# Kernel tuning notes

Measured on AMD Instinct MI355X. Metric: run time of the kernel, lower is better.

Reference implementation:

```python
import jax, jax.numpy as jnp
import numpy as np

DIM = 128
HEADS = 8
DH = DIM // HEADS
WIN = (4, 4, 4)
TOPK = 4
EPS = 1e-6


def _ln(x, g, b):
    mu = jnp.mean(x, -1, keepdims=True)
    var = jnp.mean((x - mu) ** 2, -1, keepdims=True)
    return (x - mu) * jax.lax.rsqrt(var + EPS) * g + b


def _win3d(x, p1, p2, p3):
    # x: [B,S,H,W,C] -> [B, p1*p2*p3, Ms, Mh, Mw, C]
    B, S, H, W, C = x.shape
    Ms, Mh, Mw = S // p1, H // p2, W // p3
    x = x.reshape(B, p1, Ms, p2, Mh, p3, Mw, C)
    x = x.transpose(0, 1, 3, 5, 2, 4, 6, 7)
    return x.reshape(B, p1 * p2 * p3, Ms, Mh, Mw, C)


def setup_inputs() -> dict:
    key = jax.random.key(0)
    ks = jax.random.split(key, 20)

    def lin(k, din, dout):
        return jax.random.normal(k, (din, dout), jnp.float32) * 0.02

    return {
        "x_in": jax.random.normal(ks[0], (2, 128, 16, 32, 32), jnp.float32),
        "x_g_in": jax.random.normal(ks[1], (2, 128, 8, 16, 16), jnp.float32),
        # Atten (global branch)
        "qkv_w": lin(ks[2], DIM, 3 * DIM), "qkv_b": jnp.zeros((3 * DIM,), jnp.float32),
        "proj_w": lin(ks[3], DIM, DIM), "proj_b": jnp.zeros((DIM,), jnp.float32),
        # shared LayerNorm (self.norm1 is reused everywhere in the original)
        "ln_g": jnp.ones((DIM,), jnp.float32), "ln_b": jnp.zeros((DIM,), jnp.float32),
        # mlp (global branch FFN)
        "mlp_w1": lin(ks[4], DIM, 4 * DIM), "mlp_b1": jnp.zeros((4 * DIM,), jnp.float32),
        "mlp_w2": lin(ks[5], 4 * DIM, DIM), "mlp_b2": jnp.zeros((DIM,), jnp.float32),
        # TopkRouting
        "rq_w": lin(ks[6], DIM, DIM), "rq_b": jnp.zeros((DIM,), jnp.float32),
        "rk_w": lin(ks[7], DIM, DIM), "rk_b": jnp.zeros((DIM,), jnp.float32),
        # fused qkv over concatenated local+gathered-global tokens
        "gqkv_w": lin(ks[8], DIM, 3 * DIM), "gqkv_b": jnp.zeros((3 * DIM,), jnp.float32),
        "wo_w": lin(ks[9], DIM, DIM), "wo_b": jnp.zeros((DIM,), jnp.float32),
        # mlp2 (local branch FFN)
        "mlp2_w1": lin(ks[10], DIM, 4 * DIM), "mlp2_b1": jnp.zeros((4 * DIM,), jnp.float32),
        "mlp2_w2": lin(ks[11], 4 * DIM, DIM), "mlp2_b2": jnp.zeros((DIM,), jnp.float32),
    }


def reference(x_in, x_g_in, qkv_w, qkv_b, proj_w, proj_b, ln_g, ln_b,
              mlp_w1, mlp_b1, mlp_w2, mlp_b2, rq_w, rq_b, rk_w, rk_b,
              gqkv_w, gqkv_b, wo_w, wo_b, mlp2_w1, mlp2_b1, mlp2_w2, mlp2_b2):
    B, C, S, H, W = x_in.shape
    Ms, Mh, Mw = WIN
    p1, p2, p3 = S // Ms, H // Mh, W // Mw  # pads are zero for these shapes
    nw, w3l = p1 * p2 * p3, Ms * Mh * Mw
    scale = DIM ** -0.5  # BiLevelRoutingAttention.scale = dim**-0.5 (not per-head)

    x = jnp.transpose(x_in, (0, 2, 3, 4, 1))  # [B,S,H,W,C]
    shortcut_l = _win3d(x, p1, p2, p3).reshape(B, nw, w3l, C)

    # ---- global branch: full self-attention + FFN ----
    _, _, gS, gH, gW = x_g_in.shape
    gN = gS * gH * gW
    xg = jnp.transpose(x_g_in, (0, 2, 3, 4, 1)).reshape(B, gN, C)
    h = _ln(xg, ln_g, ln_b)
    qkv = (h @ qkv_w + qkv_b).reshape(B, gN, 3, HEADS, DH).transpose(2, 0, 3, 1, 4)
    q, k, v = qkv[0], qkv[1], qkv[2]
    a = jax.nn.softmax(jnp.einsum('bhnd,bhmd->bhnm', q, k) * DH ** -0.5, axis=-1)
    o = jnp.einsum('bhnm,bhmd->bhnd', a, v).transpose(0, 2, 1, 3).reshape(B, gN, C)
    xg = (o @ proj_w + proj_b) + xg
    xg4 = xg.reshape(B, gS, gH, gW, C)
    h = _ln(xg4, ln_g, ln_b)
    xg4 = xg4 + (jax.nn.gelu(h @ mlp_w1 + mlp_b1, approximate=False) @ mlp_w2 + mlp_b2)

    # ---- top-k window routing ----
    swg = _win3d(xg4, p1, p2, p3)  # [B,nw,gMs,gMh,gMw,C]
    w3g = swg.shape[2] * swg.shape[3] * swg.shape[4]
    g_win = swg.mean((2, 3, 4))  # [B,nw,C]
    qh = g_win @ rq_w + rq_b
    kh = g_win @ rk_w + rk_b
    logit = jnp.einsum('bnc,bmc->bnm', qh * scale, kh)
    _tvals, tidx = jax.lax.top_k(logit, TOPK)  # r_weight is computed but unused in the original forward

    # gather top-k global windows' tokens per local window
    gflat = swg.reshape(B, nw, w3g, C)
    gath = jax.vmap(lambda kv, idx: kv[idx])(gflat, tidx)  # [B,nw,topk,w3g,C]
    sc = jnp.concatenate([shortcut_l, gath.reshape(B, nw, TOPK * w3g, C)], axis=2)
    w3 = w3l + TOPK * w3g

    # ---- local+routed attention over concatenated tokens ----
    qkvp = _ln(sc, ln_g, ln_b) @ gqkv_w + gqkv_b
    qp, kp, vp = jnp.split(qkvp, 3, axis=-1)
    qp = qp.reshape(B, nw, w3, HEADS, DH)
    kp = kp.reshape(B, nw, w3, HEADS, DH)
    vp = vp.reshape(B, nw, w3, HEADS, DH)
    aw = jax.nn.softmax(jnp.einsum('bnqhd,bnkhd->bnhqk', qp * scale, kp), axis=-1)
    out = jnp.einsum('bnhqk,bnkhd->bnqhd', aw, vp).reshape(B, nw, w3, C)

    l = out[:, :, :w3l] @ wo_w + wo_b + shortcut_l
    l = l.reshape(B, p1, p2, p3, Ms, Mh, Mw, C).transpose(0, 1, 4, 2, 5, 3, 6, 7).reshape(B, S, H, W, C)
    l = l + (jax.nn.gelu(_ln(l, ln_g, ln_b) @ mlp2_w1 + mlp2_b1, approximate=False) @ mlp2_w2 + mlp2_b2)

    l_out = jnp.transpose(l, (0, 4, 1, 2, 3))
    g_out = jnp.transpose(xg4, (0, 4, 1, 2, 3))
    return (l_out, g_out)
```

## Files before the change

kernel.cpp:

```cpp
#include <hip/hip_runtime.h>
#include <hip/hip_bf16.h>
#include <math.h>

#define BATCH 2
#define CDIM 128
#define SS 16
#define HH_ 32
#define WW_ 32
#define NSP (SS*HH_*WW_)
#define GS 8
#define GH 16
#define GW 16
#define GN (GS*GH*GW)
#define HEADS 8
#define DH 16
#define NW 256
#define W3L 64
#define W3G 8
#define TOPK 4
#define W3 (W3L + TOPK*W3G)
#define LN_EPS 1e-6f
#define ROUTE_SCALE 0.08838834764831845f
#define GATTN_SCALE 0.25f

typedef short bshort8 __attribute__((ext_vector_type(8)));
typedef float f32x4 __attribute__((ext_vector_type(4)));

__device__ __forceinline__ unsigned short f2bf(float f) {
    unsigned int u = __float_as_uint(f);
    unsigned int r = (u + 0x7fffu + ((u >> 16) & 1u)) >> 16;
    return (unsigned short)r;
}
__device__ __forceinline__ float gelu_exact(float x) {
    return 0.5f * x * (1.0f + erff(x * 0.70710678118654752f));
}
__device__ __forceinline__ float shfl_sum32(float v) {
#pragma unroll
    for (int m = 16; m > 0; m >>= 1) v += __shfl_xor(v, m);
    return v;
}
__device__ __forceinline__ float shfl_sum16(float v) {
#pragma unroll
    for (int m = 8; m > 0; m >>= 1) v += __shfl_xor(v, m);
    return v;
}
__device__ __forceinline__ float shfl_sum8(float v) {
#pragma unroll
    for (int m = 4; m > 0; m >>= 1) v += __shfl_xor(v, m);
    return v;
}

__global__ __launch_bounds__(256) void k_wprep_all(const float* __restrict__ gqkv_w,
        const float* __restrict__ m2_w1, const float* __restrict__ m2_w2,
        const float* __restrict__ proj_w, const float* __restrict__ mlp_w1,
        const float* __restrict__ mlp_w2, const float* __restrict__ wo_w,
        const float* __restrict__ qkv_w,
        unsigned short* __restrict__ wt, unsigned short* __restrict__ w1t,
        unsigned short* __restrict__ w2t, unsigned short* __restrict__ projt,
        unsigned short* __restrict__ gw1t, unsigned short* __restrict__ gw2t,
        unsigned short* __restrict__ wot, unsigned short* __restrict__ qkvt) {
    int id = blockIdx.x * 256 + threadIdx.x;
    if (id < 49152) {
        int n = id >> 7, k = id & 127;
        float v = gqkv_w[k * 384 + n];
        if (n < 128) v *= ROUTE_SCALE;
        wt[id] = f2bf(v);
    } else if (id < 114688) {
        int i = id - 49152; int n = i >> 7, k = i & 127;
        w1t[i] = f2bf(m2_w1[k * 512 + n]);
    } else if (id < 180224) {
        int i = id - 114688; int n = i >> 9, k = i & 511;
        w2t[i] = f2bf(m2_w2[k * 128 + n]);
    } else if (id < 196608) {
        int i = id - 180224; int n = i >> 7, k = i & 127;
        projt[i] = f2bf(proj_w[k * 128 + n]);
    } else if (id < 262144) {
        int i = id - 196608; int n = i >> 7, k = i & 127;
        gw1t[i] = f2bf(mlp_w1[k * 512 + n]);
    } else if (id < 327680) {
        int i = id - 262144; int n = i >> 9, k = i & 511;
        gw2t[i] = f2bf(mlp_w2[k * 128 + n]);
    } else if (id < 344064) {
        int i = id - 327680; int n = i >> 7, k = i & 127;
        wot[i] = f2bf(wo_w[k * 128 + n]);
    } else {
        int i = id - 344064; int n = i >> 7, k = i & 127;
        float v = qkv_w[k * 384 + n];
        if (n < 128) v *= GATTN_SCALE;
        qkvt[i] = f2bf(v);
    }
}

__global__ __launch_bounds__(256) void k_gqkv_mfma(const float* __restrict__ xg_in,
        const unsigned short* __restrict__ qkvt, const float* __restrict__ qkv_b,
        const float* __restrict__ ln_g, const float* __restrict__ ln_b,
        float* __restrict__ xg, unsigned short* __restrict__ qgb,
        unsigned short* __restrict__ kgb, unsigned short* __restrict__ vgtb) {
    int blk = blockIdx.x; int b = blk >> 7; int n0 = (blk & 127) * 16;
    int t = threadIdx.x; int w = t >> 6; int lane = t & 63;
    int l15 = lane & 15, quad = lane >> 4;
    __shared__ __align__(16) float xs[16 * 132];
    __shared__ __align__(16) unsigned short h[16 * 136];
    f32x4 zero4 = {0.f, 0.f, 0.f, 0.f};

    {
        int c = t >> 1, j0 = (t & 1) * 8;
        const float* src = xg_in + ((size_t)(b * 128 + c)) * GN + n0 + j0;
        float4 v0 = *(const float4*)src;
        float4 v1 = *(const float4*)(src + 4);
        xs[(j0 + 0) * 132 + c] = v0.x; xs[(j0 + 1) * 132 + c] = v0.y;
        xs[(j0 + 2) * 132 + c] = v0.z; xs[(j0 + 3) * 132 + c] = v0.w;
        xs[(j0 + 4) * 132 + c] = v1.x; xs[(j0 + 5) * 132 + c] = v1.y;
        xs[(j0 + 6) * 132 + c] = v1.z; xs[(j0 + 7) * 132 + c] = v1.w;
    }
    __syncthreads();
    {
        int j = t >> 4, p = t & 15, c0 = p * 8;
        float vv[8]; float s1 = 0.f;
#pragma unroll
        for (int i = 0; i < 8; i++) { vv[i] = xs[j * 132 + c0 + i]; s1 += vv[i]; }
        s1 = shfl_sum16(s1);
        float mu = s1 * (1.0f / 128.0f);
        float s2 = 0.f;
#pragma unroll
        for (int i = 0; i < 8; i++) { float d = vv[i] - mu; s2 += d * d; }
        s2 = shfl_sum16(s2);
        float rs = rsqrtf(s2 * (1.0f / 128.0f) + LN_EPS);
        float* dst = xg + ((size_t)(b * GN) + n0 + j) * 128 + c0;
        *(float4*)dst = *(float4*)&vv[0];
        *(float4*)(dst + 4) = *(float4*)&vv[4];
        unsigned short hb[8];
#pragma unroll
        for (int i4 = 0; i4 < 2; i4++) {
            float4 g4 = *(const float4*)(ln_g + c0 + i4 * 4);
            float4 b4 = *(const float4*)(ln_b + c0 + i4 * 4);
            hb[i4 * 4 + 0] = f2bf((vv[i4 * 4 + 0] - mu) * rs * g4.x + b4.x);
            hb[i4 * 4 + 1] = f2bf((vv[i4 * 4 + 1] - mu) * rs * g4.y + b4.y);
            hb[i4 * 4 + 2] = f2bf((vv[i4 * 4 + 2] - mu) * rs * g4.z + b4.z);
            hb[i4 * 4 + 3] = f2bf((vv[i4 * 4 + 3] - mu) * rs * g4.w + b4.w);
        }
        *(ushort4*)&h[j * 136 + c0] = *(ushort4*)&hb[0];
        *(ushort4*)&h[j * 136 + c0 + 4] = *(ushort4*)&hb[4];
    }
    __syncthreads();

    bshort8 a[4];
#pragma unroll
    for (int ks = 0; ks < 4; ks++)
        a[ks] = *(const bshort8*)(h + l15 * 136 + ks * 32 + quad * 8);
    int bh_base = b * HEADS;
#pragma unroll
    for (int part = 0; part < 2; part++) {
#pragma unroll
        for (int which = 0; which < 2; which++) {
            int nt = 2 * w + which;
            int ncol = part * 128 + nt * 16;
            f32x4 acc = zero4;
#pragma unroll
            for (int ks = 0; ks < 4; ks++) {
                bshort8 bfr = *(const bshort8*)(qkvt + (size_t)(ncol + l15) * 128 + ks * 32 + quad * 8);
                acc = __builtin_amdgcn_mfma_f32_16x16x32_bf16(a[ks], bfr, acc, 0, 0, 0);
            }
            float bias = qkv_b[ncol + l15] * (part == 0 ? GATTN_SCALE : 1.f);
            unsigned short* dst = (part == 0) ? qgb : kgb;
#pragma unroll
            for (int r = 0; r < 4; r++)
                dst[((size_t)(bh_base + nt) * GN + n0 + quad * 4 + r) * DH + l15] = f2bf(acc[r] + bias);
        }
    }
#pragma unroll
    for (int which = 0; which < 2; which++) {
        int mtv = 2 * w + which;
        f32x4 acc = zero4;
#pragma unroll
        for (int ks = 0; ks < 4; ks++) {
            bshort8 aw = *(const bshort8*)(qkvt + (size_t)(256 + mtv * 16 + l15) * 128 + ks * 32 + quad * 8);
            acc = __builtin_amdgcn_mfma_f32_16x16x32_bf16(aw, a[ks], acc, 0, 0, 0);
        }
#pragma unroll
        for (int r = 0; r < 4; r++) {
            float bias = qkv_b[256 + mtv * 16 + quad * 4 + r];
            vgtb[((size_t)(bh_base + mtv) * DH + quad * 4 + r) * GN + n0 + l15] = f2bf(acc[r] + bias);
        }
    }
}

__global__ __launch_bounds__(256) void k_gattn_mfma(const unsigned short* __restrict__ qgb,
        const unsigned short* __restrict__ kgb, const unsigned short* __restrict__ vgtb,
        float* __restrict__ og) {
    int blk = blockIdx.x;
    int bh = blk >> 7; int qt = (blk & 127) << 4;
    int b = bh >> 3, hh = bh & 7;
    int t = threadIdx.x; int w = t >> 6; int lane = t & 63;
    int col = lane & 15, quad = lane >> 4;
    __shared__ __align__(16) unsigned short Pbuf[4 * 16 * 40];
    __shared__ float po[4][64][4];
    __shared__ float pl[4][64][4];

    bshort8 aq = {0, 0, 0, 0, 0, 0, 0, 0};
    if (quad < 2)
        aq = *(const bshort8*)(qgb + ((size_t)bh * GN + qt + col) * DH + quad * 8);

    f32x4 o = {0.f, 0.f, 0.f, 0.f};
    float lsum[4] = {0.f, 0.f, 0.f, 0.f};
    const unsigned short* kb = kgb + (size_t)bh * GN * DH;
    const unsigned short* vb = vgtb + (size_t)bh * DH * GN;
    unsigned short* pb = Pbuf + w * (16 * 40);
    int row0 = quad * 4;
    int kbeg = w * 512;
    for (int kc = kbeg; kc < kbeg + 512; kc += 32) {
        bshort8 bk0 = {0, 0, 0, 0, 0, 0, 0, 0};
        bshort8 bk1 = {0, 0, 0, 0, 0, 0, 0, 0};
        if (quad < 2) {
            bk0 = *(const bshort8*)(kb + (size_t)(kc + col) * DH + quad * 8);
            bk1 = *(const bshort8*)(kb + (size_t)(kc + 16 + col) * DH + quad * 8);
        }
        f32x4 z = {0.f, 0.f, 0.f, 0.f};
        f32x4 s0 = __builtin_amdgcn_mfma_f32_16x16x32_bf16(aq, bk0, z, 0, 0, 0);
        f32x4 s1 = __builtin_amdgcn_mfma_f32_16x16x32_bf16(aq, bk1, z, 0, 0, 0);
        float p0[4], p1[4];
#pragma unroll
        for (int r = 0; r < 4; r++) {
            p0[r] = __expf(s0[r]); p1[r] = __expf(s1[r]);
            lsum[r] += p0[r] + p1[r];
        }
#pragma unroll
        for (int r = 0; r < 4; r++) {
            pb[(row0 + r) * 40 + col] = f2bf(p0[r]);
            pb[(row0 + r) * 40 + 16 + col] = f2bf(p1[r]);
        }
        bshort8 pA = *(const bshort8*)(pb + col * 40 + quad * 8);
        bshort8 bv = *(const bshort8*)(vb + (size_t)col * GN + kc + quad * 8);
        o = __builtin_amdgcn_mfma_f32_16x16x32_bf16(pA, bv, o, 0, 0, 0);
    }
#pragma unroll
    for (int r = 0; r < 4; r++) {
        float v = lsum[r];
        v += __shfl_xor(v, 1); v += __shfl_xor(v, 2);
        v += __shfl_xor(v, 4); v += __shfl_xor(v, 8);
        lsum[r] = v;
    }
#pragma unroll
    for (int r = 0; r < 4; r++) { po[w][lane][r] = o[r]; pl[w][lane][r] = lsum[r]; }
    __syncthreads();
    if (w == 0) {
#pragma unroll
        for (int r = 0; r < 4; r++) {
            float os = po[0][lane][r] + po[1][lane][r] + po[2][lane][r] + po[3][lane][r];
            float ls = pl[0][lane][r] + pl[1][lane][r] + pl[2][lane][r] + pl[3][lane][r];
            og[((size_t)(b * GN) + qt + quad * 4 + r) * 128 + hh * 16 + col] = os / ls;
        }
    }
}

__global__ __launch_bounds__(256) void k_gmlp_mfma(const float* __restrict__ og,
        const float* __restrict__ xg,
        const unsigned short* __restrict__ projt, const float* __restrict__ proj_b,
        const float* __restrict__ ln_g, const float* __restrict__ ln_b,
        const unsigned short* __restrict__ gw1t, const float* __restrict__ b1,
        const unsigned short* __restrict__ gw2t, const float* __restrict__ b2,
        float* __restrict__ xg4, float* __restrict__ gout) {
    int blk = blockIdx.x; int b = blk >> 7; int n0g = (blk & 127) * 16;
    int t = threadIdx.x; int w = t >> 6; int lane = t & 63;
    int l15 = lane & 15, quad = lane >> 4;
    __shared__ __align__(16) unsigned short ao[16 * 136];
    __shared__ __align__(16) float xs[16 * 132];
    __shared__ __align__(16) unsigned short h[16 * 136];
    __shared__ __align__(16) unsigned short h1[16 * 520];
    float* of32 = (float*)h1;
    f32x4 zero4 = {0.f, 0.f, 0.f, 0.f};

    {
        int j = t >> 4, p = t & 15, c0 = p * 8;
        size_t base = ((size_t)(b * GN) + n0g + j) * 128 + c0;
        float4 v0 = *(const float4*)(og + base);
        float4 v1 = *(const float4*)(og + base + 4);
        ushort4 u0 = { f2bf(v0.x), f2bf(v0.y), f2bf(v0.z), f2bf(v0.w) };
        ushort4 u1 = { f2bf(v1.x), f2bf(v1.y), f2bf(v1.z), f2bf(v1.w) };
        *(ushort4*)&ao[j * 136 + c0] = u0;
        *(ushort4*)&ao[j * 136 + c0 + 4] = u1;
        *(float4*)&xs[j * 132 + c0] = *(const float4*)(xg + base);
        *(float4*)&xs[j * 132 + c0 + 4] = *(const float4*)(xg + base + 4);
    }
    __syncthreads();

    {
        bshort8 a[4];
#pragma unroll
        for (int ks = 0; ks < 4; ks++)
            a[ks] = *(const bshort8*)(ao + l15 * 136 + ks * 32 + quad * 8);
#pragma unroll
        for (int nt = 0; nt < 2; nt++) {
            int n0 = w * 32 + nt * 16;
            f32x4 acc = zero4;
#pragma unroll
            for (int ks = 0; ks < 4; ks++) {
                bshort8 bfr = *(const bshort8*)(projt + (n0 + l15) * 128 + ks * 32 + quad * 8);
                acc = __builtin_amdgcn_mfma_f32_16x16x32_bf16(a[ks], bfr, acc, 0, 0, 0);
            }
            float bias = proj_b[n0 + l15];
#pragma unroll
            for (int r = 0; r < 4; r++) {
                int m = quad * 4 + r;
                xs[m * 132 + n0 + l15] += acc[r] + bias;
            }
        }
    }
    __syncthreads();

    {
        int j = t >> 4, p = t & 15, c0 = p * 8;
        float vv[8]; float s1 = 0.f;
#pragma unroll
        for (int i = 0; i < 8; i++) { vv[i] = xs[j * 132 + c0 + i]; s1 += vv[i]; }
        s1 = shfl_sum16(s1);
        float mu = s1 * (1.0f / 128.0f);
        float s2 = 0.f;
#pragma unroll
        for (int i = 0; i < 8; i++) { float d = vv[i] - mu; s2 += d * d; }
        s2 = shfl_sum16(s2);
        float rs = rsqrtf(s2 * (1.0f / 128.0f) + LN_EPS);
        unsigned short hb[8];
#pragma unroll
        for (int i4 = 0; i4 < 2; i4++) {
            float4 g4 = *(const float4*)(ln_g + c0 + i4 * 4);
            float4 b4 = *(const float4*)(ln_b + c0 + i4 * 4);
            hb[i4 * 4 + 0] = f2bf((vv[i4 * 4 + 0] - mu) * rs * g4.x + b4.x);
            hb[i4 * 4 + 1] = f2bf((vv[i4 * 4 + 1] - mu) * rs * g4.y + b4.y);
            hb[i4 * 4 + 2] = f2bf((vv[i4 * 4 + 2] - mu) * rs * g4.z + b4.z);
            hb[i4 * 4 + 3] = f2bf((vv[i4 * 4 + 3] - mu) * rs * g4.w + b4.w);
        }
        *(ushort4*)&h[j * 136 + c0] = *(ushort4*)&hb[0];
        *(ushort4*)&h[j * 136 + c0 + 4] = *(ushort4*)&hb[4];
    }
    __syncthreads();

    {
        bshort8 a[4];
#pragma unroll
        for (int ks = 0; ks < 4; ks++)
            a[ks] = *(const bshort8*)(h + l15 * 136 + ks * 32 + quad * 8);
#pragma unroll
        for (int nt = 0; nt < 8; nt++) {
            int n0 = w * 128 + nt * 16;
            f32x4 acc = zero4;
#pragma unroll
            for (int ks = 0; ks < 4; ks++) {
                bshort8 bfr = *(const bshort8*)(gw1t + (size_t)(n0 + l15) * 128 + ks * 32 + quad * 8);
                acc = __builtin_amdgcn_mfma_f32_16x16x32_bf16(a[ks], bfr, acc, 0, 0, 0);
            }
            float bias = b1[n0 + l15];
#pragma unroll
            for (int r = 0; r < 4; r++)
                h1[(quad * 4 + r) * 520 + n0 + l15] = f2bf(gelu_exact(acc[r] + bias));
        }
    }
    __syncthreads();

    f32x4 acc2[2]; acc2[0] = zero4; acc2[1] = zero4;
#pragma unroll 4
    for (int ks = 0; ks < 16; ks++) {
        bshort8 a = *(const bshort8*)(h1 + l15 * 520 + ks * 32 + quad * 8);
#pragma unroll
        for (int nt = 0; nt < 2; nt++) {
            int n0 = w * 32 + nt * 16;
            bshort8 bfr = *(const bshort8*)(gw2t + (size_t)(n0 + l15) * 512 + ks * 32 + quad * 8);
            acc2[nt] = __builtin_amdgcn_mfma_f32_16x16x32_bf16(a, bfr, acc2[nt], 0, 0, 0);
        }
    }
    __syncthreads();

    {
#pragma unroll
        for (int nt = 0; nt < 2; nt++) {
            int n0 = w * 32 + nt * 16;
            float bias = b2[n0 + l15];
#pragma unroll
            for (int r = 0; r < 4; r++) {
                int m = quad * 4 + r;
                float ov = xs[m * 132 + n0 + l15] + acc2[nt][r] + bias;
                of32[m * 132 + n0 + l15] = ov;
                xg4[((size_t)(b * GN) + n0g + m) * 128 + n0 + l15] = ov;
            }
        }
    }
    __syncthreads();

    {
        int cw = t >> 1, hf = t & 1, j0 = hf * 8;
        float* dst = gout + ((size_t)(b * 128 + cw)) * GN + n0g + j0;
#pragma unroll
        for (int i4 = 0; i4 < 2; i4++) {
            float4 ov = { of32[(j0 + i4 * 4 + 0) * 132 + cw], of32[(j0 + i4 * 4 + 1) * 132 + cw],
                          of32[(j0 + i4 * 4 + 2) * 132 + cw], of32[(j0 + i4 * 4 + 3) * 132 + cw] };
            *(float4*)(dst + i4 * 4) = ov;
        }
    }
}

__global__ void k_routing_qk(const float* __restrict__ xg4,
                             const float* __restrict__ rq_w, const float* __restrict__ rq_b,
                             const float* __restrict__ rk_w, const float* __restrict__ rk_b,
                             float* __restrict__ qh, float* __restrict__ kh) {
    int wid = blockIdx.x; int b = wid / NW, n = wid % NW;
    int c = threadIdx.x;
    int i1 = n / 64, i2 = (n / 8) % 8, i3 = n % 8;
    __shared__ float g[CDIM];
    float s = 0.f;
#pragma unroll
    for (int j = 0; j < W3G; j++) {
        int ds = j >> 2, dh = (j >> 1) & 1, dw = j & 1;
        int gi = ((i1 * 2 + ds) * GH + (i2 * 2 + dh)) * GW + (i3 * 2 + dw);
        s += xg4[((size_t)(b * GN + gi)) * CDIM + c];
    }
    g[c] = s * (1.0f / W3G);
    __syncthreads();
    float aq = rq_b[c], ak = rk_b[c];
    for (int k = 0; k < CDIM; k++) { float gv = g[k]; aq = fmaf(gv, rq_w[k * CDIM + c], aq); ak = fmaf(gv, rk_w[k * CDIM + c], ak); }
    qh[(size_t)wid * CDIM + c] = aq;
    kh[(size_t)wid * CDIM + c] = ak;
}

__global__ void k_topk(const float* __restrict__ qh, const float* __restrict__ kh,
                       int* __restrict__ tidx) {
    int wid = blockIdx.x; int b = wid / NW;
    int m = threadIdx.x;
    __shared__ float q[CDIM];
    __shared__ float lv[NW];
    __shared__ int li[NW];
    if (m < CDIM) q[m] = qh[(size_t)wid * CDIM + m] * ROUTE_SCALE;
    __syncthreads();
    float acc = 0.f;
    const float* kr = kh + ((size_t)b * NW + m) * CDIM;
    for (int k = 0; k < CDIM; k++) acc = fmaf(q[k], kr[k], acc);
#pragma unroll
    for (int sel = 0; sel < TOPK; sel++) {
        lv[m] = acc; li[m] = m; __syncthreads();
#pragma unroll
        for (int s = 128; s > 0; s >>= 1) {
            if (m < s) {
                if (lv[m + s] > lv[m] || (lv[m + s] == lv[m] && li[m + s] < li[m])) {
                    lv[m] = lv[m + s]; li[m] = li[m + s];
                }
            }
            __syncthreads();
        }
        int best = li[0]; __syncthreads();
        if (m == best) acc = -1e30f;
        if (m == 0) tidx[wid * TOPK + sel] = best;
    }
}

__global__ __launch_bounds__(256) void k_lnsc_local(const float* __restrict__ x_in,
        const float* __restrict__ ln_g, const float* __restrict__ ln_b,
        unsigned short* __restrict__ lnsc) {
    int blk = blockIdx.x;
    int wt = blk & 1; int hh = (blk >> 1) & 31; int s = (blk >> 6) & 15; int b = blk >> 10;
    int w0 = wt * 16;
    int t = threadIdx.x;
    __shared__ float tile[16][132];
    {
        int c = t >> 1; int wq = (t & 1) * 8;
        const float* src = x_in + (((size_t)(b * 128 + c) * SS + s)) * 1024 + hh * 32 + w0 + wq;
        float4 v0 = *(const float4*)src;
        float4 v1 = *(const float4*)(src + 4);
        tile[wq + 0][c] = v0.x; tile[wq + 1][c] = v0.y; tile[wq + 2][c] = v0.z; tile[wq + 3][c] = v0.w;
        tile[wq + 4][c] = v1.x; tile[wq + 5][c] = v1.y; tile[wq + 6][c] = v1.z; tile[wq + 7][c] = v1.w;
    }
    __syncthreads();
    int w = t >> 4; int j = t & 15;
    float vals[8];
    float s1 = 0.f;
#pragma unroll
    for (int i = 0; i < 8; i++) { vals[i] = tile[w][j * 8 + i]; s1 += vals[i]; }
    s1 = shfl_sum16(s1);
    float mu = s1 * (1.0f / 128.0f);
    float s2 = 0.f;
#pragma unroll
    for (int i = 0; i < 8; i++) { float d = vals[i] - mu; s2 += d * d; }
    s2 = shfl_sum16(s2);
    float rs = rsqrtf(s2 * (1.0f / 128.0f) + LN_EPS);
    float4 g0 = *(const float4*)(ln_g + j * 8);
    float4 g1 = *(const float4*)(ln_g + j * 8 + 4);
    float4 b0 = *(const float4*)(ln_b + j * 8);
    float4 b1 = *(const float4*)(ln_b + j * 8 + 4);
    float gv[8] = { g0.x, g0.y, g0.z, g0.w, g1.x, g1.y, g1.z, g1.w };
    float bv[8] = { b0.x, b0.y, b0.z, b0.w, b1.x, b1.y, b1.z, b1.w };
    int ww = w0 + w;
    int n = (s >> 2) * 64 + (hh >> 2) * 8 + (ww >> 2);
    int slot = (s & 3) * 16 + (hh & 3) * 4 + (ww & 3);
    unsigned short* dst = lnsc + ((size_t)(b * NW + n) * W3 + slot) * 128 + j * 8;
    ushort4 u0, u1;
    u0.x = f2bf((vals[0] - mu) * rs * gv[0] + bv[0]);
    u0.y = f2bf((vals[1] - mu) * rs * gv[1] + bv[1]);
    u0.z = f2bf((vals[2] - mu) * rs * gv[2] + bv[2]);
    u0.w = f2bf((vals[3] - mu) * rs * gv[3] + bv[3]);
    u1.x = f2bf((vals[4] - mu) * rs * gv[4] + bv[4]);
    u1.y = f2bf((vals[5] - mu) * rs * gv[5] + bv[5]);
    u1.z = f2bf((vals[6] - mu) * rs * gv[6] + bv[6]);
    u1.w = f2bf((vals[7] - mu) * rs * gv[7] + bv[7]);
    *(ushort4*)dst = u0;
    *(ushort4*)(dst + 4) = u1;
}

__global__ __launch_bounds__(256) void k_lnsc_gath(const float* __restrict__ xg4,
        const int* __restrict__ tidx,
        const float* __restrict__ ln_g, const float* __restrict__ ln_b,
        unsigned short* __restrict__ lnsc) {
    int blk = blockIdx.x;
    int kk = blk & 3; int wn = blk >> 2;
    int b = wn >> 8;
    int g = tidx[wn * TOPK + kk];
    int gi1 = g >> 6, gi2 = (g >> 3) & 7, gi3 = g & 7;
    int t = threadIdx.x; int j = t >> 5, lj = t & 31;
    int ds = j >> 2, dh = (j >> 1) & 1, dw = j & 1;
    int gi = ((gi1 * 2 + ds) * GH + (gi2 * 2 + dh)) * GW + (gi3 * 2 + dw);
    float4 v = *(const float4*)(xg4 + ((size_t)(b * GN + gi)) * 128 + lj * 4);
    float s1 = shfl_sum32(v.x + v.y + v.z + v.w);
    float mu = s1 * (1.0f / 128.0f);
    float d0 = v.x - mu, d1 = v.y - mu, d2 = v.z - mu, d3 = v.w - mu;
    float s2 = shfl_sum32(d0 * d0 + d1 * d1 + d2 * d2 + d3 * d3);
    float rs = rsqrtf(s2 * (1.0f / 128.0f) + LN_EPS);
    float4 g4 = *(const float4*)(ln_g + lj * 4);
    float4 b4 = *(const float4*)(ln_b + lj * 4);
    ushort4 u;
    u.x = f2bf(d0 * rs * g4.x + b4.x);
    u.y = f2bf(d1 * rs * g4.y + b4.y);
    u.z = f2bf(d2 * rs * g4.z + b4.z);
    u.w = f2bf(d3 * rs * g4.w + b4.w);
    *(ushort4*)(lnsc + ((size_t)wn * W3 + 64 + kk * 8 + j) * 128 + lj * 4) = u;
}

__global__ __launch_bounds__(512, 4) void k_local_mfma(const unsigned short* __restrict__ lnsc,
        const unsigned short* __restrict__ wt, const float* __restrict__ gqkv_b,
        float* __restrict__ aout) {
    int wn = blockIdx.x;
    int t = threadIdx.x; int w = t >> 6; int lane = t & 63;
    int l15 = lane & 15, quad = lane >> 4;
    __shared__ __align__(16) unsigned short Qs[64 * 136];
    __shared__ __align__(16) unsigned short Ks2[96 * 136];
    __shared__ __align__(16) unsigned short Vts[128 * 104];
    __shared__ __align__(16) unsigned short Ps[8][16 * 40];

    const unsigned short* Xb = lnsc + (size_t)wn * W3 * 128;
    f32x4 zero4 = {0.f, 0.f, 0.f, 0.f};

    bshort8 qw[4], kw[4], vw[4];
#pragma unroll
    for (int ks = 0; ks < 4; ks++) {
        qw[ks] = *(const bshort8*)(wt + (w * 16 + l15) * 128 + ks * 32 + quad * 8);
        kw[ks] = *(const bshort8*)(wt + (128 + w * 16 + l15) * 128 + ks * 32 + quad * 8);
        vw[ks] = *(const bshort8*)(wt + (256 + w * 16 + l15) * 128 + ks * 32 + quad * 8);
    }
    float qbias = gqkv_b[w * 16 + l15] * ROUTE_SCALE;
    float kbias = gqkv_b[128 + w * 16 + l15];
    float vbias[4];
#pragma unroll
    for (int r = 0; r < 4; r++) vbias[r] = gqkv_b[256 + w * 16 + quad * 4 + r];

    for (int mt = 0; mt < 6; mt++) {
        bshort8 a[4];
#pragma unroll
        for (int ks = 0; ks < 4; ks++)
            a[ks] = *(const bshort8*)(Xb + (mt * 16 + l15) * 128 + ks * 32 + quad * 8);
        f32x4 acck = zero4;
        f32x4 accv = zero4;
#pragma unroll
        for (int ks = 0; ks < 4; ks++) {
            acck = __builtin_amdgcn_mfma_f32_16x16x32_bf16(a[ks], kw[ks], acck, 0, 0, 0);
            accv = __builtin_amdgcn_mfma_f32_16x16x32_bf16(vw[ks], a[ks], accv, 0, 0, 0);
        }
#pragma unroll
        for (int r = 0; r < 4; r++) {
            Ks2[(mt * 16 + quad * 4 + r) * 136 + w * 16 + l15] = f2bf(acck[r] + kbias);
            Vts[(w * 16 + quad * 4 + r) * 104 + mt * 16 + l15] = f2bf(accv[r] + vbias[r]);
        }
        if (mt < 4) {
            f32x4 accq = zero4;
#pragma unroll
            for (int ks = 0; ks < 4; ks++)
                accq = __builtin_amdgcn_mfma_f32_16x16x32_bf16(a[ks], qw[ks], accq, 0, 0, 0);
#pragma unroll
            for (int r = 0; r < 4; r++)
                Qs[(mt * 16 + quad * 4 + r) * 136 + w * 16 + l15] = f2bf(accq[r] + qbias);
        }
    }

    unsigned short* Pw = &Ps[w][0];
    bshort8 zfrag = {0, 0, 0, 0, 0, 0, 0, 0};
    int h = w;
    for (int mt = 0; mt < 4; mt++) {
        bshort8 aq = zfrag;
        if (quad < 2)
            aq = *(const bshort8*)(Qs + (mt * 16 + l15) * 136 + h * 16 + quad * 8);
        float rsum[4] = {0.f, 0.f, 0.f, 0.f};
        f32x4 oacc = zero4;
#pragma unroll
        for (int kc = 0; kc < 96; kc += 32) {
#pragma unroll
            for (int sub = 0; sub < 2; sub++) {
                int nt = (kc >> 4) + sub;
                bshort8 bk = zfrag;
                if (quad < 2)
                    bk = *(const bshort8*)(Ks2 + (nt * 16 + l15) * 136 + h * 16 + quad * 8);
                f32x4 s = __builtin_amdgcn_mfma_f32_16x16x32_bf16(aq, bk, zero4, 0, 0, 0);
#pragma unroll
                for (int r = 0; r < 4; r++) {
                    float p = __expf(s[r]);
                    rsum[r] += p;
                    Pw[(quad * 4 + r) * 40 + sub * 16 + l15] = f2bf(p);
                }
            }
            bshort8 ap = *(const bshort8*)(Pw + l15 * 40 + quad * 8);
            bshort8 bv = *(const bshort8*)(Vts + (h * 16 + l15) * 104 + kc + quad * 8);
            oacc = __builtin_amdgcn_mfma_f32_16x16x32_bf16(ap, bv, oacc, 0, 0, 0);
        }
#pragma unroll
        for (int r = 0; r < 4; r++) {
            float v = rsum[r];
            v += __shfl_xor(v, 1); v += __shfl_xor(v, 2);
            v += __shfl_xor(v, 4); v += __shfl_xor(v, 8);
            rsum[r] = v;
        }
#pragma unroll
        for (int r = 0; r < 4; r++)
            aout[((size_t)wn * W3L + mt * 16 + quad * 4 + r) * 128 + h * 16 + l15]
                = oacc[r] / rsum[r];
    }
}

__global__ __launch_bounds__(256) void k_wo_mfma(const float* __restrict__ aout,
        const unsigned short* __restrict__ wot, const float* __restrict__ wo_b,
        const float* __restrict__ x_in, float* __restrict__ lpre) {
    int blk = blockIdx.x; int T0 = blk * 32;
    int b = T0 >> 14; int sp0 = T0 & 16383;
    int t = threadIdx.x; int w = t >> 6; int lane = t & 63;
    int l15 = lane & 15, quad = lane >> 4;
    __shared__ __align__(16) unsigned short as2[32 * 136];
    __shared__ __align__(16) float xs[32 * 132];
    f32x4 zero4 = {0.f, 0.f, 0.f, 0.f};

    {
        int j = t >> 3, p = t & 7, c0 = p * 16;
        int sp = sp0 + j;
        int s = sp >> 10, hh = (sp >> 5) & 31, ww = sp & 31;
        int n = (s >> 2) * 64 + (hh >> 2) * 8 + (ww >> 2);
        int slot = (s & 3) * 16 + (hh & 3) * 4 + (ww & 3);
        const float* src = aout + (((size_t)(b * NW + n)) * W3L + slot) * 128 + c0;
#pragma unroll
        for (int i4 = 0; i4 < 4; i4++) {
            float4 v = *(const float4*)(src + i4 * 4);
            ushort4 u = { f2bf(v.x), f2bf(v.y), f2bf(v.z), f2bf(v.w) };
            *(ushort4*)&as2[j * 136 + c0 + i4 * 4] = u;
        }
    }
    {
        int c = t >> 1, half = t & 1, j0 = half * 16;
        const float* src = x_in + ((size_t)(b * 128 + c)) * 16384 + sp0 + j0;
#pragma unroll
        for (int i4 = 0; i4 < 4; i4++) {
            float4 v = *(const float4*)(src + i4 * 4);
            xs[(j0 + i4 * 4 + 0) * 132 + c] = v.x;
            xs[(j0 + i4 * 4 + 1) * 132 + c] = v.y;
            xs[(j0 + i4 * 4 + 2) * 132 + c] = v.z;
            xs[(j0 + i4 * 4 + 3) * 132 + c] = v.w;
        }
    }
    __syncthreads();

    bshort8 a[2][4];
#pragma unroll
    for (int mt = 0; mt < 2; mt++)
#pragma unroll
        for (int ks = 0; ks < 4; ks++)
            a[mt][ks] = *(const bshort8*)(as2 + (mt * 16 + l15) * 136 + ks * 32 + quad * 8);
#pragma unroll
    for (int nt = 0; nt < 2; nt++) {
        int n0 = w * 32 + nt * 16;
        f32x4 acc0 = zero4, acc1 = zero4;
#pragma unroll
        for (int ks = 0; ks < 4; ks++) {
            bshort8 bfr = *(const bshort8*)(wot + (n0 + l15) * 128 + ks * 32 + quad * 8);
            acc0 = __builtin_amdgcn_mfma_f32_16x16x32_bf16(a[0][ks], bfr, acc0, 0, 0, 0);
            acc1 = __builtin_amdgcn_mfma_f32_16x16x32_bf16(a[1][ks], bfr, acc1, 0, 0, 0);
        }
        float bias = wo_b[n0 + l15];
#pragma unroll
        for (int r = 0; r < 4; r++) {
            int m0 = quad * 4 + r;
            int m1 = 16 + quad * 4 + r;
            lpre[((size_t)T0 + m0) * 128 + n0 + l15] = acc0[r] + bias + xs[m0 * 132 + n0 + l15];
            lpre[((size_t)T0 + m1) * 128 + n0 + l15] = acc1[r] + bias + xs[m1 * 132 + n0 + l15];
        }
    }
}

__global__ __launch_bounds__(256) void k_mlp2_mfma(const float* __restrict__ lpre,
        const float* __restrict__ ln_g, const float* __restrict__ ln_b,
        const unsigned short* __restrict__ w1t, const float* __restrict__ b1,
        const unsigned short* __restrict__ w2t, const float* __restrict__ b2,
        float* __restrict__ lout) {
    int blk = blockIdx.x;
    int T0 = blk * 32;
    int b = T0 >> 14;
    int sp = T0 & 16383;
    int t = threadIdx.x; int w = t >> 6; int lane = t & 63;
    int l15 = lane & 15, quad = lane >> 4;
    __shared__ __align__(16) unsigned short buf[32 * 520];
    float* of32 = (float*)buf;

    {
        int j = t >> 3, p = t & 7, c0 = p * 16;
        const float* src = lpre + ((size_t)T0 + j) * 128 + c0;
        float4 v0 = *(const float4*)(src + 0);
        float4 v1 = *(const float4*)(src + 4);
        float4 v2 = *(const float4*)(src + 8);
        float4 v3 = *(const float4*)(src + 12);
        float s1 = (v0.x + v0.y + v0.z + v0.w) + (v1.x + v1.y + v1.z + v1.w)
                 + (v2.x + v2.y + v2.z + v2.w) + (v3.x + v3.y + v3.z + v3.w);
        s1 = shfl_sum8(s1);
        float mu = s1 * (1.0f / 128.0f);
        float vv[16] = { v0.x, v0.y, v0.z, v0.w, v1.x, v1.y, v1.z, v1.w,
                         v2.x, v2.y, v2.z, v2.w, v3.x, v3.y, v3.z, v3.w };
        float s2 = 0.f;
#pragma unroll
        for (int i = 0; i < 16; i++) { float d = vv[i] - mu; s2 += d * d; }
        s2 = shfl_sum8(s2);
        float rs = rsqrtf(s2 * (1.0f / 128.0f) + LN_EPS);
        unsigned short hb[16];
#pragma unroll
        for (int i4 = 0; i4 < 4; i4++) {
            float4 g4 = *(const float4*)(ln_g + c0 + i4 * 4);
            float4 b4 = *(const float4*)(ln_b + c0 + i4 * 4);
            hb[i4 * 4 + 0] = f2bf((vv[i4 * 4 + 0] - mu) * rs * g4.x + b4.x);
            hb[i4 * 4 + 1] = f2bf((vv[i4 * 4 + 1] - mu) * rs * g4.y + b4.y);
            hb[i4 * 4 + 2] = f2bf((vv[i4 * 4 + 2] - mu) * rs * g4.z + b4.z);
            hb[i4 * 4 + 3] = f2bf((vv[i4 * 4 + 3] - mu) * rs * g4.w + b4.w);
        }
        *(ushort4*)&buf[j * 136 + c0 + 0] = *(ushort4*)&hb[0];
        *(ushort4*)&buf[j * 136 + c0 + 4] = *(ushort4*)&hb[4];
        *(ushort4*)&buf[j * 136 + c0 + 8] = *(ushort4*)&hb[8];
        *(ushort4*)&buf[j * 136 + c0 + 12] = *(ushort4*)&hb[12];
    }
    __syncthreads();

    bshort8 a1[2][4];
#pragma unroll
    for (int mt = 0; mt < 2; mt++)
#pragma unroll
        for (int ks = 0; ks < 4; ks++)
            a1[mt][ks] = *(const bshort8*)(buf + (mt * 16 + l15) * 136 + ks * 32 + quad * 8);
    __syncthreads();

    f32x4 zero4 = {0.f, 0.f, 0.f, 0.f};
    {
        int n0w = w * 128;
#pragma unroll
        for (int nt = 0; nt < 8; nt++) {
            int n0 = n0w + nt * 16;
            f32x4 acc0 = zero4, acc1 = zero4;
#pragma unroll
            for (int ks = 0; ks < 4; ks++) {
                bshort8 bfr = *(const bshort8*)(w1t + (size_t)(n0 + l15) * 128 + ks * 32 + quad * 8);
                acc0 = __builtin_amdgcn_mfma_f32_16x16x32_bf16(a1[0][ks], bfr, acc0, 0, 0, 0);
                acc1 = __builtin_amdgcn_mfma_f32_16x16x32_bf16(a1[1][ks], bfr, acc1, 0, 0, 0);
            }
            float bias = b1[n0 + l15];
#pragma unroll
            for (int r = 0; r < 4; r++) {
                buf[(quad * 4 + r) * 520 + n0 + l15] = f2bf(gelu_exact(acc0[r] + bias));
                buf[(16 + quad * 4 + r) * 520 + n0 + l15] = f2bf(gelu_exact(acc1[r] + bias));
            }
        }
    }
    __syncthreads();

    f32x4 acc[2][2];
    acc[0][0] = zero4; acc[0][1] = zero4; acc[1][0] = zero4; acc[1][1] = zero4;
    {
#pragma unroll 4
        for (int ks = 0; ks < 16; ks++) {
            bshort8 a0 = *(const bshort8*)(buf + (l15) * 520 + ks * 32 + quad * 8);
            bshort8 a1b = *(const bshort8*)(buf + (16 + l15) * 520 + ks * 32 + quad * 8);
#pragma unroll
            for (int nt = 0; nt < 2; nt++) {
                int n0 = w * 32 + nt * 16;
                bshort8 bfr = *(const bshort8*)(w2t + (size_t)(n0 + l15) * 512 + ks * 32 + quad * 8);
                acc[0][nt] = __builtin_amdgcn_mfma_f32_16x16x32_bf16(a0, bfr, acc[0][nt], 0, 0, 0);
                acc[1][nt] = __builtin_amdgcn_mfma_f32_16x16x32_bf16(a1b, bfr, acc[1][nt], 0, 0, 0);
            }
        }
    }
    __syncthreads();

#pragma unroll
    for (int mt = 0; mt < 2; mt++) {
#pragma unroll
        for (int nt = 0; nt < 2; nt++) {
            int n0 = w * 32 + nt * 16;
            float bias = b2[n0 + l15];
#pragma unroll
            for (int r = 0; r < 4; r++) {
                int m = mt * 16 + quad * 4 + r;
                float res = lpre[((size_t)T0 + m) * 128 + n0 + l15];
                of32[m * 132 + n0 + l15] = res + acc[mt][nt][r] + bias;
            }
        }
    }
    __syncthreads();

    {
        int c = t >> 1, half = t & 1, j0 = half * 16;
        float* dst = lout + ((size_t)(b * 128 + c)) * NSP + sp + j0;
#pragma unroll
        for (int i4 = 0; i4 < 4; i4++) {
            float4 ov = { of32[(j0 + i4 * 4 + 0) * 132 + c], of32[(j0 + i4 * 4 + 1) * 132 + c],
                          of32[(j0 + i4 * 4 + 2) * 132 + c], of32[(j0 + i4 * 4 + 3) * 132 + c] };
            *(float4*)(dst + i4 * 4) = ov;
        }
    }
}

extern "C" void kernel_launch(void* const* d_in, const int* in_sizes, int n_in,
                              void* d_out, int out_size, void* d_ws, size_t ws_size,
                              hipStream_t stream) {
    const float* x_in   = (const float*)d_in[0];
    const float* xg_in  = (const float*)d_in[1];
    const float* qkv_w  = (const float*)d_in[2];
    const float* qkv_b  = (const float*)d_in[3];
    const float* proj_w = (const float*)d_in[4];
    const float* proj_b = (const float*)d_in[5];
    const float* ln_g   = (const float*)d_in[6];
    const float* ln_b   = (const float*)d_in[7];
    const float* mlp_w1 = (const float*)d_in[8];
    const float* mlp_b1 = (const float*)d_in[9];
    const float* mlp_w2 = (const float*)d_in[10];
    const float* mlp_b2 = (const float*)d_in[11];
    const float* rq_w   = (const float*)d_in[12];
    const float* rq_b   = (const float*)d_in[13];
    const float* rk_w   = (const float*)d_in[14];
    const float* rk_b   = (const float*)d_in[15];
    const float* gqkv_w = (const float*)d_in[16];
    const float* gqkv_b = (const float*)d_in[17];
    const float* wo_w   = (const float*)d_in[18];
    const float* wo_b   = (const float*)d_in[19];
    const float* m2_w1  = (const float*)d_in[20];
    const float* m2_b1  = (const float*)d_in[21];
    const float* m2_w2  = (const float*)d_in[22];
    const float* m2_b2  = (const float*)d_in[23];

    float* out = (float*)d_out;
    float* ws  = (float*)d_ws;

    float* xg4 = ws;
    float* xg  = ws + 524288;
    unsigned short* qgb  = (unsigned short*)(ws + 1048576);
    unsigned short* kgb  = (unsigned short*)(ws + 1310720);
    unsigned short* vgtb = (unsigned short*)(ws + 1572864);
    float* og  = ws + 1835008;
    float* qh  = ws + 2359296;
    float* kh  = ws + 2424832;
    int*   tidx = (int*)(ws + 2490368);
    unsigned short* lnsc = (unsigned short*)(ws + 2492416);
    float* aout = ws + 2492416 + 3145728;
    float* lpre = ws + 9832448;
    unsigned short* wt   = (unsigned short*)(ws + 14026752);
    unsigned short* w1t  = (unsigned short*)(ws + 14051328);
    unsigned short* w2t  = (unsigned short*)(ws + 14084096);
    unsigned short* projt = (unsigned short*)(ws + 14116864);
    unsigned short* gw1t  = (unsigned short*)(ws + 14125056);
    unsigned short* gw2t  = (unsigned short*)(ws + 14157824);
    unsigned short* wot   = (unsigned short*)(ws + 14190592);
    unsigned short* qkvt  = (unsigned short*)(ws + 14198784);

    const size_t L_OUT = (size_t)BATCH * CDIM * NSP;
    float* gout = out + L_OUT;

    hipLaunchKernelGGL(k_wprep_all, dim3(1536), dim3(256), 0, stream,
                       gqkv_w, m2_w1, m2_w2, proj_w, mlp_w1, mlp_w2, wo_w, qkv_w,
                       wt, w1t, w2t, projt, gw1t, gw2t, wot, qkvt);
    hipLaunchKernelGGL(k_gqkv_mfma, dim3(256), dim3(256), 0, stream,
                       xg_in, qkvt, qkv_b, ln_g, ln_b, xg, qgb, kgb, vgtb);
    hipLaunchKernelGGL(k_gattn_mfma, dim3(2048), dim3(256), 0, stream, qgb, kgb, vgtb, og);
    hipLaunchKernelGGL(k_gmlp_mfma, dim3(256), dim3(256), 0, stream,
                       og, xg, projt, proj_b, ln_g, ln_b, gw1t, mlp_b1, gw2t, mlp_b2,
                       xg4, gout);
    hipLaunchKernelGGL(k_routing_qk, dim3(512), dim3(128), 0, stream,
                       xg4, rq_w, rq_b, rk_w, rk_b, qh, kh);
    hipLaunchKernelGGL(k_topk, dim3(512), dim3(256), 0, stream, qh, kh, tidx);
    hipLaunchKernelGGL(k_lnsc_local, dim3(2048), dim3(256), 0, stream,
                       x_in, ln_g, ln_b, lnsc);
    hipLaunchKernelGGL(k_lnsc_gath, dim3(2048), dim3(256), 0, stream,
                       xg4, tidx, ln_g, ln_b, lnsc);
    hipLaunchKernelGGL(k_local_mfma, dim3(512), dim3(512), 0, stream,
                       lnsc, wt, gqkv_b, aout);
    hipLaunchKernelGGL(k_wo_mfma, dim3(1024), dim3(256), 0, stream,
                       aout, wot, wo_b, x_in, lpre);
    hipLaunchKernelGGL(k_mlp2_mfma, dim3(1024), dim3(256), 0, stream,
                       lpre, ln_g, ln_b, w1t, m2_b1, w2t, m2_b2, out);
}
```

Measured before the change: 268.6 us.

## Fuse Wo projection and local MLP2 into one kernel over 16-token tiles

Merges the Wo output projection (plus bias and residual) with the LayerNorm+MLP2 kernel, so the lpre intermediate stays in shared memory instead of making a global write and read round trip. The tile shrinks from 32 to 16 tokens per block, doubling the grid to keep occupancy with the larger shared footprint. In exchange each weight fragment is reused across only one M-tile, which doubles weight reads per token, and one kernel launch is removed.

After: 286.9 us. 6.8% more time.

```diff
diff --git a/kernel.cpp b/kernel.cpp
--- a/kernel.cpp
+++ b/kernel.cpp
@@ -629,107 +629,91 @@
     }
 }
 
-__global__ __launch_bounds__(256) void k_wo_mfma(const float* __restrict__ aout,
+__global__ __launch_bounds__(256) void k_wo_mlp2_fused(const float* __restrict__ aout,
         const unsigned short* __restrict__ wot, const float* __restrict__ wo_b,
-        const float* __restrict__ x_in, float* __restrict__ lpre) {
-    int blk = blockIdx.x; int T0 = blk * 32;
-    int b = T0 >> 14; int sp0 = T0 & 16383;
+        const float* __restrict__ x_in,
+        const float* __restrict__ ln_g, const float* __restrict__ ln_b,
+        const unsigned short* __restrict__ w1t, const float* __restrict__ b1,
+        const unsigned short* __restrict__ w2t, const float* __restrict__ b2,
+        float* __restrict__ lout) {
+    int blk = blockIdx.x;
+    int T0 = blk * 16;
+    int b = T0 >> 14;
+    int sp0 = T0 & 16383;
     int t = threadIdx.x; int w = t >> 6; int lane = t & 63;
     int l15 = lane & 15, quad = lane >> 4;
-    __shared__ __align__(16) unsigned short as2[32 * 136];
-    __shared__ __align__(16) float xs[32 * 132];
+    __shared__ __align__(16) float xs[16 * 132];
+    __shared__ __align__(16) unsigned short h[16 * 136];
+    __shared__ __align__(16) unsigned short h1[16 * 520];
+    unsigned short* as2 = h1;
+    float* of32 = (float*)h1;
     f32x4 zero4 = {0.f, 0.f, 0.f, 0.f};
 
     {
-        int j = t >> 3, p = t & 7, c0 = p * 16;
+        int j = t >> 4, p = t & 15, c0 = p * 8;
         int sp = sp0 + j;
         int s = sp >> 10, hh = (sp >> 5) & 31, ww = sp & 31;
         int n = (s >> 2) * 64 + (hh >> 2) * 8 + (ww >> 2);
         int slot = (s & 3) * 16 + (hh & 3) * 4 + (ww & 3);
         const float* src = aout + (((size_t)(b * NW + n)) * W3L + slot) * 128 + c0;
-#pragma unroll
-        for (int i4 = 0; i4 < 4; i4++) {
-            float4 v = *(const float4*)(src + i4 * 4);
-            ushort4 u = { f2bf(v.x), f2bf(v.y), f2bf(v.z), f2bf(v.w) };
-            *(ushort4*)&as2[j * 136 + c0 + i4 * 4] = u;
-        }
-    }
-    {
-        int c = t >> 1, half = t & 1, j0 = half * 16;
+        float4 v0 = *(const float4*)(src);
+        float4 v1 = *(const float4*)(src + 4);
+        ushort4 u0 = { f2bf(v0.x), f2bf(v0.y), f2bf(v0.z), f2bf(v0.w) };
+        ushort4 u1 = { f2bf(v1.x), f2bf(v1.y), f2bf(v1.z), f2bf(v1.w) };
+        *(ushort4*)&as2[j * 136 + c0] = u0;
+        *(ushort4*)&as2[j * 136 + c0 + 4] = u1;
+    }
+    {
+        int c = t >> 1, half = t & 1, j0 = half * 8;
         const float* src = x_in + ((size_t)(b * 128 + c)) * 16384 + sp0 + j0;
-#pragma unroll
-        for (int i4 = 0; i4 < 4; i4++) {
-            float4 v = *(const float4*)(src + i4 * 4);
-            xs[(j0 + i4 * 4 + 0) * 132 + c] = v.x;
-            xs[(j0 + i4 * 4 + 1) * 132 + c] = v.y;
-            xs[(j0 + i4 * 4 + 2) * 132 + c] = v.z;
-            xs[(j0 + i4 * 4 + 3) * 132 + c] = v.w;
-        }
-    }
-    __syncthreads();
-
-    bshort8 a[2][4];
-#pragma unroll
-    for (int mt = 0; mt < 2; mt++)
+        float4 v0 = *(const float4*)(src);
+        float4 v1 = *(const float4*)(src + 4);
+        xs[(j0 + 0) * 132 + c] = v0.x; xs[(j0 + 1) * 132 + c] = v0.y;
+        xs[(j0 + 2) * 132 + c] = v0.z; xs[(j0 + 3) * 132 + c] = v0.w;
+        xs[(j0 + 4) * 132 + c] = v1.x; xs[(j0 + 5) * 132 + c] = v1.y;
+        xs[(j0 + 6) * 132 + c] = v1.z; xs[(j0 + 7) * 132 + c] = v1.w;
+    }
+    __syncthreads();
+
+    {
+        bshort8 a[4];
 #pragma unroll
         for (int ks = 0; ks < 4; ks++)
-            a[mt][ks] = *(const bshort8*)(as2 + (mt * 16 + l15) * 136 + ks * 32 + quad * 8);
-#pragma unroll
-    for (int nt = 0; nt < 2; nt++) {
-        int n0 = w * 32 + nt * 16;
-        f32x4 acc0 = zero4, acc1 = zero4;
-#pragma unroll
-        for (int ks = 0; ks < 4; ks++) {
-            bshort8 bfr = *(const bshort8*)(wot + (n0 + l15) * 128 + ks * 32 + quad * 8);
-            acc0 = __builtin_amdgcn_mfma_f32_16x16x32_bf16(a[0][ks], bfr, acc0, 0, 0, 0);
-            acc1 = __builtin_amdgcn_mfma_f32_16x16x32_bf16(a[1][ks], bfr, acc1, 0, 0, 0);
-        }
-        float bias = wo_b[n0 + l15];
-#pragma unroll
-        for (int r = 0; r < 4; r++) {
-            int m0 = quad * 4 + r;
-            int m1 = 16 + quad * 4 + r;
-            lpre[((size_t)T0 + m0) * 128 + n0 + l15] = acc0[r] + bias + xs[m0 * 132 + n0 + l15];
-            lpre[((size_t)T0 + m1) * 128 + n0 + l15] = acc1[r] + bias + xs[m1 * 132 + n0 + l15];
-        }
-    }
-}
-
-__global__ __launch_bounds__(256) void k_mlp2_mfma(const float* __restrict__ lpre,
-        const float* __restrict__ ln_g, const float* __restrict__ ln_b,
-        const unsigned short* __restrict__ w1t, const float* __restrict__ b1,
-        const unsigned short* __restrict__ w2t, const float* __restrict__ b2,
-        float* __restrict__ lout) {
-    int blk = blockIdx.x;
-    int T0 = blk * 32;
-    int b = T0 >> 14;
-    int sp = T0 & 16383;
-    int t = threadIdx.x; int w = t >> 6; int lane = t & 63;
-    int l15 = lane & 15, quad = lane >> 4;
-    __shared__ __align__(16) unsigned short buf[32 * 520];
-    float* of32 = (float*)buf;
-
-    {
-        int j = t >> 3, p = t & 7, c0 = p * 16;
-        const float* src = lpre + ((size_t)T0 + j) * 128 + c0;
-        float4 v0 = *(const float4*)(src + 0);
-        float4 v1 = *(const float4*)(src + 4);
-        float4 v2 = *(const float4*)(src + 8);
-        float4 v3 = *(const float4*)(src + 12);
-        float s1 = (v0.x + v0.y + v0.z + v0.w) + (v1.x + v1.y + v1.z + v1.w)
-                 + (v2.x + v2.y + v2.z + v2.w) + (v3.x + v3.y + v3.z + v3.w);
-        s1 = shfl_sum8(s1);
+            a[ks] = *(const bshort8*)(as2 + l15 * 136 + ks * 32 + quad * 8);
+#pragma unroll
+        for (int nt = 0; nt < 2; nt++) {
+            int n0 = w * 32 + nt * 16;
+            f32x4 acc = zero4;
+#pragma unroll
+            for (int ks = 0; ks < 4; ks++) {
+                bshort8 bfr = *(const bshort8*)(wot + (n0 + l15) * 128 + ks * 32 + quad * 8);
+                acc = __builtin_amdgcn_mfma_f32_16x16x32_bf16(a[ks], bfr, acc, 0, 0, 0);
+            }
+            float bias = wo_b[n0 + l15];
+#pragma unroll
+            for (int r = 0; r < 4; r++) {
+                int m = quad * 4 + r;
+                xs[m * 132 + n0 + l15] += acc[r] + bias;
+            }
+        }
+    }
+    __syncthreads();
+
+    {
+        int j = t >> 4, p = t & 15, c0 = p * 8;
+        float vv[8]; float s1 = 0.f;
+#pragma unroll
+        for (int i = 0; i < 8; i++) { vv[i] = xs[j * 132 + c0 + i]; s1 += vv[i]; }
+        s1 = shfl_sum16(s1);
         float mu = s1 * (1.0f / 128.0f);
-        float vv[16] = { v0.x, v0.y, v0.z, v0.w, v1.x, v1.y, v1.z, v1.w,
-                         v2.x, v2.y, v2.z, v2.w, v3.x, v3.y, v3.z, v3.w };
         float s2 = 0.f;
 #pragma unroll
-        for (int i = 0; i < 16; i++) { float d = vv[i] - mu; s2 += d * d; }
-        s2 = shfl_sum8(s2);
+        for (int i = 0; i < 8; i++) { float d = vv[i] - mu; s2 += d * d; }
+        s2 = shfl_sum16(s2);
         float rs = rsqrtf(s2 * (1.0f / 128.0f) + LN_EPS);
-        unsigned short hb[16];
-#pragma unroll
-        for (int i4 = 0; i4 < 4; i4++) {
+        unsigned short hb[8];
+#pragma unroll
+        for (int i4 = 0; i4 < 2; i4++) {
             float4 g4 = *(const float4*)(ln_g + c0 + i4 * 4);
             float4 b4 = *(const float4*)(ln_b + c0 + i4 * 4);
             hb[i4 * 4 + 0] = f2bf((vv[i4 * 4 + 0] - mu) * rs * g4.x + b4.x);
@@ -737,83 +721,65 @@
             hb[i4 * 4 + 2] = f2bf((vv[i4 * 4 + 2] - mu) * rs * g4.z + b4.z);
             hb[i4 * 4 + 3] = f2bf((vv[i4 * 4 + 3] - mu) * rs * g4.w + b4.w);
         }
-        *(ushort4*)&buf[j * 136 + c0 + 0] = *(ushort4*)&hb[0];
-        *(ushort4*)&buf[j * 136 + c0 + 4] = *(ushort4*)&hb[4];
-        *(ushort4*)&buf[j * 136 + c0 + 8] = *(ushort4*)&hb[8];
-        *(ushort4*)&buf[j * 136 + c0 + 12] = *(ushort4*)&hb[12];
-    }
-    __syncthreads();
-
-    bshort8 a1[2][4];
-#pragma unroll
-    for (int mt = 0; mt < 2; mt++)
+        *(ushort4*)&h[j * 136 + c0] = *(ushort4*)&hb[0];
+        *(ushort4*)&h[j * 136 + c0 + 4] = *(ushort4*)&hb[4];
+    }
+    __syncthreads();
+
+    {
+        bshort8 a[4];
 #pragma unroll
         for (int ks = 0; ks < 4; ks++)
-            a1[mt][ks] = *(const bshort8*)(buf + (mt * 16 + l15) * 136 + ks * 32 + quad * 8);
-    __syncthreads();
-
-    f32x4 zero4 = {0.f, 0.f, 0.f, 0.f};
-    {
-        int n0w = w * 128;
+            a[ks] = *(const bshort8*)(h + l15 * 136 + ks * 32 + quad * 8);
 #pragma unroll
         for (int nt = 0; nt < 8; nt++) {
-            int n0 = n0w + nt * 16;
-            f32x4 acc0 = zero4, acc1 = zero4;
+            int n0 = w * 128 + nt * 16;
+            f32x4 acc = zero4;
 #pragma unroll
             for (int ks = 0; ks < 4; ks++) {
                 bshort8 bfr = *(const bshort8*)(w1t + (size_t)(n0 + l15) * 128 + ks * 32 + quad * 8);
-                acc0 = __builtin_amdgcn_mfma_f32_16x16x32_bf16(a1[0][ks], bfr, acc0, 0, 0, 0);
-                acc1 = __builtin_amdgcn_mfma_f32_16x16x32_bf16(a1[1][ks], bfr, acc1, 0, 0, 0);
+                acc = __builtin_amdgcn_mfma_f32_16x16x32_bf16(a[ks], bfr, acc, 0, 0, 0);
             }
             float bias = b1[n0 + l15];
 #pragma unroll
-            for (int r = 0; r < 4; r++) {
-                buf[(quad * 4 + r) * 520 + n0 + l15] = f2bf(gelu_exact(acc0[r] + bias));
-                buf[(16 + quad * 4 + r) * 520 + n0 + l15] = f2bf(gelu_exact(acc1[r] + bias));
-            }
-        }
-    }
-    __syncthreads();
-
-    f32x4 acc[2][2];
-    acc[0][0] = zero4; acc[0][1] = zero4; acc[1][0] = zero4; acc[1][1] = zero4;
-    {
+            for (int r = 0; r < 4; r++)
+                h1[(quad * 4 + r) * 520 + n0 + l15] = f2bf(gelu_exact(acc[r] + bias));
+        }
+    }
+    __syncthreads();
+
+    f32x4 acc2[2]; acc2[0] = zero4; acc2[1] = zero4;
 #pragma unroll 4
-        for (int ks = 0; ks < 16; ks++) {
-            bshort8 a0 = *(const bshort8*)(buf + (l15) * 520 + ks * 32 + quad * 8);
-            bshort8 a1b = *(const bshort8*)(buf + (16 + l15) * 520 + ks * 32 + quad * 8);
-#pragma unroll
-            for (int nt = 0; nt < 2; nt++) {
-                int n0 = w * 32 + nt * 16;
-                bshort8 bfr = *(const bshort8*)(w2t + (size_t)(n0 + l15) * 512 + ks * 32 + quad * 8);
-                acc[0][nt] = __builtin_amdgcn_mfma_f32_16x16x32_bf16(a0, bfr, acc[0][nt], 0, 0, 0);
-                acc[1][nt] = __builtin_amdgcn_mfma_f32_16x16x32_bf16(a1b, bfr, acc[1][nt], 0, 0, 0);
-            }
-        }
-    }
-    __syncthreads();
-
-#pragma unroll
-    for (int mt = 0; mt < 2; mt++) {
+    for (int ks = 0; ks < 16; ks++) {
+        bshort8 a = *(const bshort8*)(h1 + l15 * 520 + ks * 32 + quad * 8);
+#pragma unroll
+        for (int nt = 0; nt < 2; nt++) {
+            int n0 = w * 32 + nt * 16;
+            bshort8 bfr = *(const bshort8*)(w2t + (size_t)(n0 + l15) * 512 + ks * 32 + quad * 8);
+            acc2[nt] = __builtin_amdgcn_mfma_f32_16x16x32_bf16(a, bfr, acc2[nt], 0, 0, 0);
+        }
+    }
+    __syncthreads();
+
+    {
 #pragma unroll
         for (int nt = 0; nt < 2; nt++) {
             int n0 = w * 32 + nt * 16;
             float bias = b2[n0 + l15];
 #pragma unroll
             for (int r = 0; r < 4; r++) {
-                int m = mt * 16 + quad * 4 + r;
-                float res = lpre[((size_t)T0 + m) * 128 + n0 + l15];
-                of32[m * 132 + n0 + l15] = res + acc[mt][nt][r] + bias;
-            }
-        }
-    }
-    __syncthreads();
-
-    {
-        int c = t >> 1, half = t & 1, j0 = half * 16;
-        float* dst = lout + ((size_t)(b * 128 + c)) * NSP + sp + j0;
-#pragma unroll
-        for (int i4 = 0; i4 < 4; i4++) {
+                int m = quad * 4 + r;
+                of32[m * 132 + n0 + l15] = xs[m * 132 + n0 + l15] + acc2[nt][r] + bias;
+            }
+        }
+    }
+    __syncthreads();
+
+    {
+        int c = t >> 1, half = t & 1, j0 = half * 8;
+        float* dst = lout + ((size_t)(b * 128 + c)) * NSP + sp0 + j0;
+#pragma unroll
+        for (int i4 = 0; i4 < 2; i4++) {
             float4 ov = { of32[(j0 + i4 * 4 + 0) * 132 + c], of32[(j0 + i4 * 4 + 1) * 132 + c],
                           of32[(j0 + i4 * 4 + 2) * 132 + c], of32[(j0 + i4 * 4 + 3) * 132 + c] };
             *(float4*)(dst + i4 * 4) = ov;
@@ -863,7 +829,6 @@
     int*   tidx = (int*)(ws + 2490368);
     unsigned short* lnsc = (unsigned short*)(ws + 2492416);
     float* aout = ws + 2492416 + 3145728;
-    float* lpre = ws + 9832448;
     unsigned short* wt   = (unsigned short*)(ws + 14026752);
     unsigned short* w1t  = (unsigned short*)(ws + 14051328);
     unsigned short* w2t  = (unsigned short*)(ws + 14084096);
@@ -894,8 +859,6 @@
                        xg4, tidx, ln_g, ln_b, lnsc);
     hipLaunchKernelGGL(k_local_mfma, dim3(512), dim3(512), 0, stream,
                        lnsc, wt, gqkv_b, aout);
-    hipLaunchKernelGGL(k_wo_mfma, dim3(1024), dim3(256), 0, stream,
-                       aout, wot, wo_b, x_in, lpre);
-    hipLaunchKernelGGL(k_mlp2_mfma, dim3(1024), dim3(256), 0, stream,
-                       lpre, ln_g, ln_b, w1t, m2_b1, w2t, m2_b2, out);
-}
+    hipLaunchKernelGGL(k_wo_mlp2_fused, dim3(2048), dim3(256), 0, stream,
+                       aout, wot, wo_b, x_in, ln_g, ln_b, w1t, m2_b1, w2t, m2_b2, out);
+}
```
